# Optimization experiments

Hardware: AMD Instinct MI355X
Metric: run time of the kernel (lower is better)

Reference implementation:

```python
import jax, jax.numpy as jnp
import numpy as np

N_NODES = 40000
N_EDGES = 640000
D_FEAT = 128
HIDDEN = 128
N_GRAPHS = 512


def setup_inputs() -> dict:
    key = jax.random.key(0)
    ks = jax.random.split(key, 6)
    x = jax.random.normal(ks[0], (N_NODES, D_FEAT), dtype=jnp.float32)
    edge_index = jax.random.randint(ks[1], (2, N_EDGES), 0, N_NODES, dtype=jnp.int32)
    batch = jnp.sort(jax.random.randint(ks[2], (N_NODES,), 0, N_GRAPHS, dtype=jnp.int32))
    s1 = 1.0 / np.sqrt(D_FEAT)
    s2 = 1.0 / np.sqrt(HIDDEN)
    W1 = jax.random.normal(ks[3], (D_FEAT, HIDDEN), dtype=jnp.float32) * s1
    b1 = jnp.zeros((HIDDEN,), dtype=jnp.float32)
    W2 = jax.random.normal(ks[4], (HIDDEN, HIDDEN), dtype=jnp.float32) * s2
    b2 = jnp.zeros((HIDDEN,), dtype=jnp.float32)
    Wfc = jax.random.normal(ks[5], (HIDDEN, 1), dtype=jnp.float32) * s2
    bfc = jnp.zeros((1,), dtype=jnp.float32)
    return {"x": x, "edge_index": edge_index, "batch": batch,
            "W1": W1, "b1": b1, "W2": W2, "b2": b2, "Wfc": Wfc, "bfc": bfc}


def _gcn_conv(x, edge_index, W, b):
    # PyG GCNConv: linear transform, add self-loops, symmetric deg^{-1/2} norm,
    # scatter-add messages from row (source) to col (target), then bias.
    n = x.shape[0]
    h = x @ W  # [N, H]
    row, col = edge_index[0], edge_index[1]
    ones = jnp.ones_like(col, dtype=h.dtype)
    deg = 1.0 + jax.ops.segment_sum(ones, col, num_segments=n)  # self-loop included
    dinv = jax.lax.rsqrt(deg)  # [N]
    norm = dinv[row] * dinv[col]  # [E]
    msg = h[row] * norm[:, None]  # [E, H]
    out = jax.ops.segment_sum(msg, col, num_segments=n)
    out = out + h * (dinv * dinv)[:, None]  # self-loop contribution
    return out + b


def _mean_pool(x, batch, num_graphs):
    sums = jax.ops.segment_sum(x, batch, num_segments=num_graphs)
    cnt = jax.ops.segment_sum(jnp.ones((x.shape[0],), dtype=x.dtype), batch, num_segments=num_graphs)
    return sums / jnp.maximum(cnt, 1.0)[:, None]


def reference(x, edge_index, batch, W1, b1, W2, b2, Wfc, bfc):
    h = jax.nn.relu(_gcn_conv(x, edge_index, W1, b1))
    h = jax.nn.relu(_gcn_conv(h, edge_index, W2, b2))
    g = _mean_pool(h, batch, N_GRAPHS)  # [G, H]
    return g @ Wfc + bfc  # [G, 1]
```

## Files before the change

kernel.cpp:

```cpp
#include <hip/hip_runtime.h>
#include <hip/hip_fp16.h>

#define N_NODES 40000
#define N_EDGES 640000
#define NFEAT   128
#define N_GRAPHS 512
#define SCAN_NB 157
#define NBKT    157
#define BKT_CAP 8192
#define BIN_BLK_EDGES 2048
#define NBLK_A ((N_EDGES + BIN_BLK_EDGES - 1) / BIN_BLK_EDGES)
#define EPAD_MAX (N_EDGES + 3 * N_NODES)

__global__ void init_misc_kernel(int* __restrict__ gcursor, int* __restrict__ gcnt,
                                 float* __restrict__ out, const float* __restrict__ bfc,
                                 __half* __restrict__ hsent) {
    int t = threadIdx.x;
    if (t < NBKT) gcursor[t] = 0;
    float b = bfc[0];
    for (int i = t; i < N_GRAPHS; i += 256) { gcnt[i] = 0; out[i] = b; }
    if (t < NFEAT) hsent[t] = __float2half(0.0f);
}

__global__ void batch_hist_kernel(const int* __restrict__ batch, int* __restrict__ gcnt, int n) {
    int i = blockIdx.x * blockDim.x + threadIdx.x;
    if (i < n) atomicAdd(&gcnt[batch[i]], 1);
}

__global__ __launch_bounds__(256) void bin_kernel(const int* __restrict__ ei,
                                                  int* __restrict__ gcursor,
                                                  unsigned int* __restrict__ binned) {
    __shared__ int lhist[NBKT];
    __shared__ int lbase[NBKT];
    const int t  = threadIdx.x;
    const int e0 = blockIdx.x * BIN_BLK_EDGES;

    if (t < NBKT) lhist[t] = 0;
    __syncthreads();

    #pragma unroll
    for (int i = 0; i < BIN_BLK_EDGES / 256; ++i) {
        int e = e0 + i * 256 + t;
        if (e < N_EDGES) atomicAdd(&lhist[ei[N_EDGES + e] >> 8], 1);
    }
    __syncthreads();

    if (t < NBKT) { lbase[t] = atomicAdd(&gcursor[t], lhist[t]); lhist[t] = 0; }
    __syncthreads();

    #pragma unroll
    for (int i = 0; i < BIN_BLK_EDGES / 256; ++i) {
        int e = e0 + i * 256 + t;
        if (e < N_EDGES) {
            int c = ei[N_EDGES + e];
            int r = ei[e];
            int bkt = c >> 8;
            int slot = atomicAdd(&lhist[bkt], 1);
            binned[(size_t)bkt * BKT_CAP + lbase[bkt] + slot] =
                (unsigned int)r | ((unsigned int)(c & 255) << 16);
        }
    }
}

__global__ __launch_bounds__(256) void bucket_hist_kernel(const unsigned int* __restrict__ binned,
                                                          const int* __restrict__ gcursor,
                                                          float* __restrict__ dinv,
                                                          int* __restrict__ pdeg) {
    __shared__ int chist[256];
    const int b = blockIdx.x, t = threadIdx.x;
    chist[t] = 0;
    __syncthreads();
    const int cnt = gcursor[b];
    const unsigned int* src = binned + (size_t)b * BKT_CAP;
    for (int i = t; i < cnt; i += 256) atomicAdd(&chist[src[i] >> 16], 1);
    __syncthreads();
    int col = b * 256 + t;
    if (col < N_NODES) {
        int d = chist[t];
        dinv[col] = rsqrtf(1.0f + (float)d);
        pdeg[col] = (d + 3) & ~3;
    }
}

__global__ void scan1_kernel(const int* __restrict__ in, int* __restrict__ out,
                             int* __restrict__ bsums, int n) {
    __shared__ int tmp[256];
    int t = threadIdx.x;
    int i = blockIdx.x * 256 + t;
    int v = (i < n) ? in[i] : 0;
    tmp[t] = v;
    __syncthreads();
    for (int off = 1; off < 256; off <<= 1) {
        int add = (t >= off) ? tmp[t - off] : 0;
        __syncthreads();
        tmp[t] += add;
        __syncthreads();
    }
    if (i < n) out[i] = tmp[t] - v;
    if (t == 255) bsums[blockIdx.x] = tmp[255];
}

__global__ void scan2_kernel(int* __restrict__ bsums, int nb) {
    __shared__ int tmp[256];
    int t = threadIdx.x;
    int v = (t < nb) ? bsums[t] : 0;
    tmp[t] = v;
    __syncthreads();
    for (int off = 1; off < 256; off <<= 1) {
        int add = (t >= off) ? tmp[t - off] : 0;
        __syncthreads();
        tmp[t] += add;
        __syncthreads();
    }
    if (t < nb) bsums[t] = tmp[t] - v;
}

__global__ void scan3_kernel(int* __restrict__ rowptr, const int* __restrict__ bsums,
                             const int* __restrict__ pdeg, int n) {
    int i = blockIdx.x * 256 + threadIdx.x;
    if (i < n) {
        int v = rowptr[i] + bsums[blockIdx.x];
        rowptr[i] = v;
        if (i == n - 1) rowptr[n] = v + pdeg[i];
    }
}

template <typename IdxT>
__global__ __launch_bounds__(256) void bucket_scatter_kernel(const unsigned int* __restrict__ binned,
                                                             const int* __restrict__ gcursor,
                                                             const int* __restrict__ rowptr,
                                                             IdxT* __restrict__ csr) {
    __shared__ int ccur[256];
    const int b = blockIdx.x, t = threadIdx.x;
    int col = b * 256 + t;
    ccur[t] = (col < N_NODES) ? rowptr[col] : 0;
    __syncthreads();
    const int cnt = gcursor[b];
    const unsigned int* src = binned + (size_t)b * BKT_CAP;
    for (int i = t; i < cnt; i += 256) {
        unsigned int u = src[i];
        int slot = atomicAdd(&ccur[u >> 16], 1);
        csr[slot] = (IdxT)(u & 0xFFFFu);
    }
    __syncthreads();
    if (col < N_NODES) {
        int end = rowptr[col + 1];
        for (int p = ccur[t]; p < end; ++p) csr[p] = (IdxT)N_NODES;
    }
}

template <typename OutT>
__global__ __launch_bounds__(256, 4) void gemm64_kernel(const float* __restrict__ X,
                                                        const float* __restrict__ W,
                                                        const float* __restrict__ dinv,
                                                        OutT* __restrict__ H) {
    __shared__ float Ws[128 * 64];
    const int colhalf = blockIdx.x & 1;
    const int tile    = blockIdx.x >> 1;

    for (int i = threadIdx.x; i < 2048; i += 256) {
        int k   = i >> 4;
        int cc4 = (i & 15) * 4;
        *(float4*)(Ws + k * 64 + cc4) = *(const float4*)(W + k * 128 + colhalf * 64 + cc4);
    }
    __syncthreads();

    const int rg = threadIdx.x >> 4;
    const int cg = threadIdx.x & 15;
    const int row0 = tile * 64 + rg * 4;
    const float* x0 = X + (size_t)row0 * NFEAT;

    float acc[4][4] = {};
    float4 xc[4], xn[4];
    #pragma unroll
    for (int i = 0; i < 4; i++) xc[i] = *(const float4*)(x0 + (size_t)i * NFEAT);

    #pragma unroll 4
    for (int k = 0; k < 128; k += 4) {
        const int kn = (k + 4) & 127;
        #pragma unroll
        for (int i = 0; i < 4; i++) xn[i] = *(const float4*)(x0 + (size_t)i * NFEAT + kn);

        float4 wv[4];
        #pragma unroll
        for (int m = 0; m < 4; m++) wv[m] = *(const float4*)(Ws + (k + m) * 64 + cg * 4);

        #pragma unroll
        for (int i = 0; i < 4; i++) {
            const float xi[4] = {xc[i].x, xc[i].y, xc[i].z, xc[i].w};
            #pragma unroll
            for (int m = 0; m < 4; m++) {
                acc[i][0] += xi[m] * wv[m].x;
                acc[i][1] += xi[m] * wv[m].y;
                acc[i][2] += xi[m] * wv[m].z;
                acc[i][3] += xi[m] * wv[m].w;
            }
        }
        #pragma unroll
        for (int i = 0; i < 4; i++) xc[i] = xn[i];
    }

    #pragma unroll
    for (int i = 0; i < 4; i++) {
        float dr = dinv[row0 + i];
        float v0 = acc[i][0] * dr, v1 = acc[i][1] * dr;
        float v2 = acc[i][2] * dr, v3 = acc[i][3] * dr;
        size_t off = (size_t)(row0 + i) * NFEAT + colhalf * 64 + cg * 4;
        if constexpr (sizeof(OutT) == 2) {
            __half2 p0 = __floats2half2_rn(v0, v1);
            __half2 p1 = __floats2half2_rn(v2, v3);
            uint2 pk;
            pk.x = *(unsigned int*)&p0;
            pk.y = *(unsigned int*)&p1;
            *(uint2*)((__half*)H + off) = pk;
        } else {
            float4 o = {v0, v1, v2, v3};
            *(float4*)((float*)H + off) = o;
        }
    }
}

__device__ inline float4 load_h4(const __half* p) {
    uint2 raw = *(const uint2*)p;
    __half2 h0 = *(__half2*)&raw.x;
    __half2 h1 = *(__half2*)&raw.y;
    float2 f0 = __half22float2(h0);
    float2 f1 = __half22float2(h1);
    return make_float4(f0.x, f0.y, f1.x, f1.y);
}

template <typename IdxT, typename IdxV, bool FUSE_POOL>
__global__ __launch_bounds__(256) void gather_h16_kernel(
        const int* __restrict__ rowptr, const IdxT* __restrict__ csr,
        const float* __restrict__ dinv, const __half* __restrict__ Ht,
        const float* __restrict__ bias, float* __restrict__ out,
        const float* __restrict__ Wfc, float* __restrict__ nodedot, int n) {
    int gid  = blockIdx.x * blockDim.x + threadIdx.x;
    int node = gid >> 6;
    if (node >= n) return;
    int lane = threadIdx.x & 63;
    int half = lane >> 5;
    int f4   = (lane & 31) * 4;

    int start = rowptr[node];
    int end   = rowptr[node + 1];

    float4 a0 = {0.f, 0.f, 0.f, 0.f};
    float4 a1 = {0.f, 0.f, 0.f, 0.f};
    if (half == 0) a0 = load_h4(Ht + (size_t)node * NFEAT + f4);

    for (int j = start; j < end; j += 4) {
        IdxV rr = *(const IdxV*)(csr + j);
        int r0 = half ? (int)rr.z : (int)rr.x;
        int r1 = half ? (int)rr.w : (int)rr.y;
        float4 v0 = load_h4(Ht + (size_t)r0 * NFEAT + f4);
        float4 v1 = load_h4(Ht + (size_t)r1 * NFEAT + f4);
        a0.x += v0.x; a0.y += v0.y; a0.z += v0.z; a0.w += v0.w;
        a1.x += v1.x; a1.y += v1.y; a1.z += v1.z; a1.w += v1.w;
    }
    a0.x += a1.x; a0.y += a1.y; a0.z += a1.z; a0.w += a1.w;

    a0.x += __shfl_xor(a0.x, 32, 64);
    a0.y += __shfl_xor(a0.y, 32, 64);
    a0.z += __shfl_xor(a0.z, 32, 64);
    a0.w += __shfl_xor(a0.w, 32, 64);

    if (half == 0) {
        float di  = dinv[node];
        float4 bb = *(const float4*)(bias + f4);
        float4 o;
        o.x = fmaxf(a0.x * di + bb.x, 0.0f);
        o.y = fmaxf(a0.y * di + bb.y, 0.0f);
        o.z = fmaxf(a0.z * di + bb.z, 0.0f);
        o.w = fmaxf(a0.w * di + bb.w, 0.0f);
        if (!FUSE_POOL) {
            *(float4*)(out + (size_t)node * NFEAT + f4) = o;
        } else {
            float4 wf = *(const float4*)(Wfc + f4);
            float d = o.x * wf.x + o.y * wf.y + o.z * wf.z + o.w * wf.w;
            d += __shfl_xor(d, 1, 64);
            d += __shfl_xor(d, 2, 64);
            d += __shfl_xor(d, 4, 64);
            d += __shfl_xor(d, 8, 64);
            d += __shfl_xor(d, 16, 64);
            if (lane == 0) nodedot[node] = d;
        }
    }
}

__global__ void pool_final_kernel(const float* __restrict__ nodedot,
                                  const int* __restrict__ batch,
                                  const int* __restrict__ gcnt,
                                  float* __restrict__ out, int n) {
    int i = blockIdx.x * blockDim.x + threadIdx.x;
    if (i < n) {
        int g = batch[i];
        int c = gcnt[g];
        float cf = (float)(c > 0 ? c : 1);
        atomicAdd(&out[g], nodedot[i] / cf);
    }
}

__global__ void edge_deg_int_kernel(const int* __restrict__ ei, int* __restrict__ degcnt, int E) {
    int e = blockIdx.x * blockDim.x + threadIdx.x;
    if (e < E) atomicAdd(&degcnt[ei[E + e]], 1);
}

__global__ void dinv_from_int_kernel(const int* __restrict__ degcnt, float* __restrict__ dinv, int n) {
    int i = blockIdx.x * blockDim.x + threadIdx.x;
    if (i < n) dinv[i] = rsqrtf(1.0f + (float)degcnt[i]);
}

__global__ __launch_bounds__(256) void edge_scatter_kernel(const int* __restrict__ ei,
                                                           const float* __restrict__ dinv,
                                                           const float* __restrict__ H,
                                                           float* __restrict__ agg,
                                                           int E) {
    long long gid = (long long)blockIdx.x * blockDim.x + threadIdx.x;
    int e = (int)(gid >> 5);
    if (e >= E) return;
    int c4 = ((int)gid & 31) * 4;
    int r = ei[e];
    int c = ei[E + e];
    float norm = dinv[c];
    const float4 hv = *(const float4*)(H + (size_t)r * NFEAT + c4);
    float* dst = agg + (size_t)c * NFEAT + c4;
    atomicAdd(dst + 0, hv.x * norm);
    atomicAdd(dst + 1, hv.y * norm);
    atomicAdd(dst + 2, hv.z * norm);
    atomicAdd(dst + 3, hv.w * norm);
}

__global__ void post_kernel(float* __restrict__ agg, const float* __restrict__ H,
                            const float* __restrict__ dinv, const float* __restrict__ b,
                            int n) {
    int gid = blockIdx.x * blockDim.x + threadIdx.x;
    if (gid >= n * 32) return;
    int node = gid >> 5;
    int c4 = (gid & 31) * 4;
    float s = dinv[node];
    float4 a  = *(float4*)(agg + (size_t)gid * 4);
    float4 hv = *(const float4*)(H + (size_t)gid * 4);
    float4 bb = *(const float4*)(b + c4);
    float4 o;
    o.x = fmaxf(a.x + hv.x * s + bb.x, 0.0f);
    o.y = fmaxf(a.y + hv.y * s + bb.y, 0.0f);
    o.z = fmaxf(a.z + hv.z * s + bb.z, 0.0f);
    o.w = fmaxf(a.w + hv.w * s + bb.w, 0.0f);
    *(float4*)(agg + (size_t)gid * 4) = o;
}

__global__ __launch_bounds__(128) void pool_fc_kernel(const float* __restrict__ H,
                                                      const int* __restrict__ batch,
                                                      const float* __restrict__ Wfc,
                                                      const float* __restrict__ bfc,
                                                      float* __restrict__ out, int n) {
    int g = blockIdx.x;
    int tid = threadIdx.x;
    int lo = 0, hi = n;
    while (lo < hi) { int mid = (lo + hi) >> 1; if (batch[mid] < g) lo = mid + 1; else hi = mid; }
    int start = lo;
    hi = n;
    while (lo < hi) { int mid = (lo + hi) >> 1; if (batch[mid] < g + 1) lo = mid + 1; else hi = mid; }
    int end = lo;

    float acc = 0.0f;
    for (int nd = start; nd < end; ++nd) acc += H[(size_t)nd * NFEAT + tid];
    float cnt = (float)((end - start) > 0 ? (end - start) : 1);
    float v = (acc / cnt) * Wfc[tid];

    __shared__ float red[128];
    red[tid] = v;
    __syncthreads();
    #pragma unroll
    for (int s = 64; s > 0; s >>= 1) {
        if (tid < s) red[tid] += red[tid + s];
        __syncthreads();
    }
    if (tid == 0) out[g] = red[0] + bfc[0];
}

template <typename IdxT, typename IdxV>
static void run_csr_path(const float* x, const int* ei, const int* batch,
                         const float* W1, const float* b1, const float* W2,
                         const float* b2, const float* Wfc, const float* bfc,
                         float* out, void* d_ws, hipStream_t stream) {
    char* ws = (char*)d_ws;
    const size_t hbytes = (size_t)(N_NODES + 1) * NFEAT * sizeof(__half);
    const size_t obytes = (size_t)N_NODES * NFEAT * sizeof(float);
    __half* hbuf  = (__half*)ws;
    float*  obuf  = (float*)(ws + hbytes);
    IdxT*   csr   = (IdxT*)(ws + hbytes + obytes);
    char*   p     = ws + hbytes + obytes + ((size_t)EPAD_MAX * sizeof(IdxT) + 15) / 16 * 16;
    int*    rowptr = (int*)p;                p += ((size_t)(N_NODES + 1) * 4 + 15) / 16 * 16;
    float*  dinv   = (float*)p;              p += ((size_t)N_NODES * 4 + 15) / 16 * 16;
    int*    gcnt   = (int*)p;

    unsigned int* binned = (unsigned int*)obuf;
    int* pdeg    = (int*)obuf + NBKT * BKT_CAP;
    int* bsums   = pdeg + N_NODES;
    int* gcursor = bsums + SCAN_NB;
    float* nodedot = (float*)obuf;

    init_misc_kernel<<<1, 256, 0, stream>>>(gcursor, gcnt, out, bfc,
                                            hbuf + (size_t)N_NODES * NFEAT);
    batch_hist_kernel<<<SCAN_NB, 256, 0, stream>>>(batch, gcnt, N_NODES);
    bin_kernel<<<NBLK_A, 256, 0, stream>>>(ei, gcursor, binned);
    bucket_hist_kernel<<<NBKT, 256, 0, stream>>>(binned, gcursor, dinv, pdeg);
    scan1_kernel<<<SCAN_NB, 256, 0, stream>>>(pdeg, rowptr, bsums, N_NODES);
    scan2_kernel<<<1, 256, 0, stream>>>(bsums, SCAN_NB);
    scan3_kernel<<<SCAN_NB, 256, 0, stream>>>(rowptr, bsums, pdeg, N_NODES);
    bucket_scatter_kernel<IdxT><<<NBKT, 256, 0, stream>>>(binned, gcursor, rowptr, csr);

    gemm64_kernel<__half><<<(N_NODES / 64) * 2, 256, 0, stream>>>(x, W1, dinv, hbuf);
    gather_h16_kernel<IdxT, IdxV, false><<<(N_NODES * 64) / 256, 256, 0, stream>>>(
        rowptr, csr, dinv, hbuf, b1, obuf, nullptr, nullptr, N_NODES);

    gemm64_kernel<__half><<<(N_NODES / 64) * 2, 256, 0, stream>>>(obuf, W2, dinv, hbuf);
    gather_h16_kernel<IdxT, IdxV, true><<<(N_NODES * 64) / 256, 256, 0, stream>>>(
        rowptr, csr, dinv, hbuf, b2, nullptr, Wfc, nodedot, N_NODES);

    pool_final_kernel<<<SCAN_NB, 256, 0, stream>>>(nodedot, batch, gcnt, out, N_NODES);
}

extern "C" void kernel_launch(void* const* d_in, const int* in_sizes, int n_in,
                              void* d_out, int out_size, void* d_ws, size_t ws_size,
                              hipStream_t stream) {
    const float* x     = (const float*)d_in[0];
    const int*   ei    = (const int*)  d_in[1];
    const int*   batch = (const int*)  d_in[2];
    const float* W1    = (const float*)d_in[3];
    const float* b1    = (const float*)d_in[4];
    const float* W2    = (const float*)d_in[5];
    const float* b2    = (const float*)d_in[6];
    const float* Wfc   = (const float*)d_in[7];
    const float* bfc   = (const float*)d_in[8];
    float* out = (float*)d_out;

    const size_t hbytes = (size_t)(N_NODES + 1) * NFEAT * sizeof(__half);
    const size_t obytes = (size_t)N_NODES * NFEAT * sizeof(float);
    const size_t tail   = ((size_t)(N_NODES + 1) * 4 + 15) / 16 * 16
                        + ((size_t)N_NODES * 4 + 15) / 16 * 16
                        + (size_t)N_GRAPHS * 4;
    const size_t needA = hbytes + obytes + ((size_t)EPAD_MAX * 4 + 15) / 16 * 16 + tail;
    const size_t needB = hbytes + obytes + ((size_t)EPAD_MAX * 2 + 15) / 16 * 16 + tail;

    if (ws_size >= needA) {
        run_csr_path<int, int4>(x, ei, batch, W1, b1, W2, b2, Wfc, bfc, out, d_ws, stream);
    } else if (ws_size >= needB) {
        run_csr_path<unsigned short, ushort4>(x, ei, batch, W1, b1, W2, b2, Wfc, bfc, out, d_ws, stream);
    } else {
        float* ws   = (float*)d_ws;
        int*   degc = (int*)ws;
        float* dinv = ws + N_NODES;
        float* hbuf = ws + 2 * N_NODES;
        float* agg  = hbuf + (size_t)N_NODES * NFEAT;
        const size_t fb2 = (size_t)N_NODES * NFEAT * sizeof(float);

        hipMemsetAsync(degc, 0, (size_t)N_NODES * sizeof(int), stream);
        edge_deg_int_kernel<<<N_EDGES / 256, 256, 0, stream>>>(ei, degc, N_EDGES);
        dinv_from_int_kernel<<<SCAN_NB, 256, 0, stream>>>(degc, dinv, N_NODES);

        hipMemsetAsync(agg, 0, fb2, stream);
        gemm64_kernel<float><<<(N_NODES / 64) * 2, 256, 0, stream>>>(x, W1, dinv, hbuf);
        edge_scatter_kernel<<<(N_EDGES * 32) / 256, 256, 0, stream>>>(ei, dinv, hbuf, agg, N_EDGES);
        post_kernel<<<(N_NODES * 32) / 256, 256, 0, stream>>>(agg, hbuf, dinv, b1, N_NODES);

        gemm64_kernel<float><<<(N_NODES / 64) * 2, 256, 0, stream>>>(agg, W2, dinv, hbuf);
        hipMemsetAsync(agg, 0, fb2, stream);
        edge_scatter_kernel<<<(N_EDGES * 32) / 256, 256, 0, stream>>>(ei, dinv, hbuf, agg, N_EDGES);
        post_kernel<<<(N_NODES * 32) / 256, 256, 0, stream>>>(agg, hbuf, dinv, b2, N_NODES);

        pool_fc_kernel<<<N_GRAPHS, 128, 0, stream>>>(agg, batch, Wfc, bfc, out, N_NODES);
    }
}
```

Before: 285.8 us.

## Fuse degree scan into bucket kernels, cache column indices, prefetch CSR indices

The local per-bucket exclusive scan of padded degrees moves into bucket_hist_kernel. A single 157-element scan kernel computes the bucket offsets, and bucket_scatter_kernel applies those offsets to rowptr and computes the padding end itself. This drops two launches and a pass over pdeg. bin_kernel keeps the column indices in registers instead of reloading them, and the gather loop prefetches the next CSR index vector one iteration ahead. The trade-off is some extra registers and a tighter coupling between the preprocessing kernels.

New measurement: 274.8 us. 1.04x faster.

```diff
diff --git a/kernel.cpp b/kernel.cpp
--- a/kernel.cpp
+++ b/kernel.cpp
@@ -38,10 +38,12 @@
     if (t < NBKT) lhist[t] = 0;
     __syncthreads();
 
+    int creg[BIN_BLK_EDGES / 256];
     #pragma unroll
     for (int i = 0; i < BIN_BLK_EDGES / 256; ++i) {
         int e = e0 + i * 256 + t;
-        if (e < N_EDGES) atomicAdd(&lhist[ei[N_EDGES + e] >> 8], 1);
+        creg[i] = (e < N_EDGES) ? ei[N_EDGES + e] : -1;
+        if (creg[i] >= 0) atomicAdd(&lhist[creg[i] >> 8], 1);
     }
     __syncthreads();
 
@@ -50,9 +52,9 @@
 
     #pragma unroll
     for (int i = 0; i < BIN_BLK_EDGES / 256; ++i) {
-        int e = e0 + i * 256 + t;
-        if (e < N_EDGES) {
-            int c = ei[N_EDGES + e];
+        int c = creg[i];
+        if (c >= 0) {
+            int e = e0 + i * 256 + t;
             int r = ei[e];
             int bkt = c >> 8;
             int slot = atomicAdd(&lhist[bkt], 1);
@@ -65,8 +67,10 @@
 __global__ __launch_bounds__(256) void bucket_hist_kernel(const unsigned int* __restrict__ binned,
                                                           const int* __restrict__ gcursor,
                                                           float* __restrict__ dinv,
-                                                          int* __restrict__ pdeg) {
+                                                          int* __restrict__ rowptr,
+                                                          int* __restrict__ bsums) {
     __shared__ int chist[256];
+    __shared__ int scn[256];
     const int b = blockIdx.x, t = threadIdx.x;
     chist[t] = 0;
     __syncthreads();
@@ -74,20 +78,27 @@
     const unsigned int* src = binned + (size_t)b * BKT_CAP;
     for (int i = t; i < cnt; i += 256) atomicAdd(&chist[src[i] >> 16], 1);
     __syncthreads();
-    int col = b * 256 + t;
-    if (col < N_NODES) {
-        int d = chist[t];
-        dinv[col] = rsqrtf(1.0f + (float)d);
-        pdeg[col] = (d + 3) & ~3;
-    }
-}
-
-__global__ void scan1_kernel(const int* __restrict__ in, int* __restrict__ out,
-                             int* __restrict__ bsums, int n) {
+    const int col = b * 256 + t;
+    const int valid = (col < N_NODES);
+    int d = chist[t];
+    if (valid) dinv[col] = rsqrtf(1.0f + (float)d);
+    int pd = valid ? ((d + 3) & ~3) : 0;
+    scn[t] = pd;
+    __syncthreads();
+    for (int off = 1; off < 256; off <<= 1) {
+        int add = (t >= off) ? scn[t - off] : 0;
+        __syncthreads();
+        scn[t] += add;
+        __syncthreads();
+    }
+    if (valid) rowptr[col] = scn[t] - pd;
+    if (t == 255) bsums[b] = scn[255];
+}
+
+__global__ void scan157_kernel(int* __restrict__ bsums, int* __restrict__ rowptr) {
     __shared__ int tmp[256];
     int t = threadIdx.x;
-    int i = blockIdx.x * 256 + t;
-    int v = (i < n) ? in[i] : 0;
+    int v = (t < NBKT) ? bsums[t] : 0;
     tmp[t] = v;
     __syncthreads();
     for (int off = 1; off < 256; off <<= 1) {
@@ -96,44 +107,26 @@
         tmp[t] += add;
         __syncthreads();
     }
-    if (i < n) out[i] = tmp[t] - v;
-    if (t == 255) bsums[blockIdx.x] = tmp[255];
-}
-
-__global__ void scan2_kernel(int* __restrict__ bsums, int nb) {
-    __shared__ int tmp[256];
-    int t = threadIdx.x;
-    int v = (t < nb) ? bsums[t] : 0;
-    tmp[t] = v;
-    __syncthreads();
-    for (int off = 1; off < 256; off <<= 1) {
-        int add = (t >= off) ? tmp[t - off] : 0;
-        __syncthreads();
-        tmp[t] += add;
-        __syncthreads();
-    }
-    if (t < nb) bsums[t] = tmp[t] - v;
-}
-
-__global__ void scan3_kernel(int* __restrict__ rowptr, const int* __restrict__ bsums,
-                             const int* __restrict__ pdeg, int n) {
-    int i = blockIdx.x * 256 + threadIdx.x;
-    if (i < n) {
-        int v = rowptr[i] + bsums[blockIdx.x];
-        rowptr[i] = v;
-        if (i == n - 1) rowptr[n] = v + pdeg[i];
-    }
+    if (t < NBKT) bsums[t] = tmp[t] - v;
+    if (t == 255) rowptr[N_NODES] = tmp[255];
 }
 
 template <typename IdxT>
 __global__ __launch_bounds__(256) void bucket_scatter_kernel(const unsigned int* __restrict__ binned,
                                                              const int* __restrict__ gcursor,
-                                                             const int* __restrict__ rowptr,
+                                                             const int* __restrict__ bsums,
+                                                             int* __restrict__ rowptr,
                                                              IdxT* __restrict__ csr) {
     __shared__ int ccur[256];
     const int b = blockIdx.x, t = threadIdx.x;
-    int col = b * 256 + t;
-    ccur[t] = (col < N_NODES) ? rowptr[col] : 0;
+    const int col = b * 256 + t;
+    const int base = bsums[b];
+    int startp = 0;
+    if (col < N_NODES) {
+        startp = rowptr[col] + base;
+        rowptr[col] = startp;
+    }
+    ccur[t] = startp;
     __syncthreads();
     const int cnt = gcursor[b];
     const unsigned int* src = binned + (size_t)b * BKT_CAP;
@@ -144,8 +137,10 @@
     }
     __syncthreads();
     if (col < N_NODES) {
-        int end = rowptr[col + 1];
-        for (int p = ccur[t]; p < end; ++p) csr[p] = (IdxT)N_NODES;
+        int cur = ccur[t];
+        int deg = cur - startp;
+        int endp = startp + ((deg + 3) & ~3);
+        for (int p = cur; p < endp; ++p) csr[p] = (IdxT)N_NODES;
     }
 }
 
@@ -249,10 +244,13 @@
     float4 a1 = {0.f, 0.f, 0.f, 0.f};
     if (half == 0) a0 = load_h4(Ht + (size_t)node * NFEAT + f4);
 
+    IdxV nxt = *(const IdxV*)(csr + start);
     for (int j = start; j < end; j += 4) {
-        IdxV rr = *(const IdxV*)(csr + j);
-        int r0 = half ? (int)rr.z : (int)rr.x;
-        int r1 = half ? (int)rr.w : (int)rr.y;
+        IdxV cur = nxt;
+        int jn = j + 4;
+        if (jn < end) nxt = *(const IdxV*)(csr + jn);
+        int r0 = half ? (int)cur.z : (int)cur.x;
+        int r1 = half ? (int)cur.w : (int)cur.y;
         float4 v0 = load_h4(Ht + (size_t)r0 * NFEAT + f4);
         float4 v1 = load_h4(Ht + (size_t)r1 * NFEAT + f4);
         a0.x += v0.x; a0.y += v0.y; a0.z += v0.z; a0.w += v0.w;
@@ -363,12 +361,10 @@
     hi = n;
     while (lo < hi) { int mid = (lo + hi) >> 1; if (batch[mid] < g + 1) lo = mid + 1; else hi = mid; }
     int end = lo;
-
     float acc = 0.0f;
     for (int nd = start; nd < end; ++nd) acc += H[(size_t)nd * NFEAT + tid];
     float cnt = (float)((end - start) > 0 ? (end - start) : 1);
     float v = (acc / cnt) * Wfc[tid];
-
     __shared__ float red[128];
     red[tid] = v;
     __syncthreads();
@@ -397,20 +393,17 @@
     int*    gcnt   = (int*)p;
 
     unsigned int* binned = (unsigned int*)obuf;
-    int* pdeg    = (int*)obuf + NBKT * BKT_CAP;
-    int* bsums   = pdeg + N_NODES;
-    int* gcursor = bsums + SCAN_NB;
+    int* bsums   = (int*)obuf + NBKT * BKT_CAP;
+    int* gcursor = bsums + NBKT;
     float* nodedot = (float*)obuf;
 
     init_misc_kernel<<<1, 256, 0, stream>>>(gcursor, gcnt, out, bfc,
                                             hbuf + (size_t)N_NODES * NFEAT);
     batch_hist_kernel<<<SCAN_NB, 256, 0, stream>>>(batch, gcnt, N_NODES);
     bin_kernel<<<NBLK_A, 256, 0, stream>>>(ei, gcursor, binned);
-    bucket_hist_kernel<<<NBKT, 256, 0, stream>>>(binned, gcursor, dinv, pdeg);
-    scan1_kernel<<<SCAN_NB, 256, 0, stream>>>(pdeg, rowptr, bsums, N_NODES);
-    scan2_kernel<<<1, 256, 0, stream>>>(bsums, SCAN_NB);
-    scan3_kernel<<<SCAN_NB, 256, 0, stream>>>(rowptr, bsums, pdeg, N_NODES);
-    bucket_scatter_kernel<IdxT><<<NBKT, 256, 0, stream>>>(binned, gcursor, rowptr, csr);
+    bucket_hist_kernel<<<NBKT, 256, 0, stream>>>(binned, gcursor, dinv, rowptr, bsums);
+    scan157_kernel<<<1, 256, 0, stream>>>(bsums, rowptr);
+    bucket_scatter_kernel<IdxT><<<NBKT, 256, 0, stream>>>(binned, gcursor, bsums, rowptr, csr);
 
     gemm64_kernel<__half><<<(N_NODES / 64) * 2, 256, 0, stream>>>(x, W1, dinv, hbuf);
     gather_h16_kernel<IdxT, IdxV, false><<<(N_NODES * 64) / 256, 256, 0, stream>>>(
```
